# Performance work log

Measured on AMD Instinct MI355X. Metric: run time of the kernel, lower is better.

## Reference

```python
import jax, jax.numpy as jnp
import numpy as np

KS = {0: (6, 18), 1: (4, 12)}


def _build_modal_edges(feat, k_set):
    # feat: [N, C] -> H_modal [N, len(k_set)*N]
    N = feat.shape[0]
    f = feat / jnp.linalg.norm(feat, axis=1, keepdims=True).clip(1e-12)
    sim = f @ f.T  # [N, N] cosine similarity
    H_list = []
    cols_base = jnp.arange(N)
    for k in k_set:
        _, knn = jax.lax.top_k(sim, k + 1)  # [N, k+1]
        rows = knn.reshape(-1)
        cols = jnp.repeat(cols_base, k + 1)
        H = jnp.zeros((N, N), dtype=feat.dtype).at[rows, cols].set(1.0)
        H_list.append(H)
    return jnp.concatenate(H_list, axis=1)


def _build_incidence(feat1, feat2):
    # feat1/feat2: [N, C] (batch-mean features) -> H [2N, 5N]
    N = feat1.shape[0]
    H1 = _build_modal_edges(feat1, KS[0])  # [N, 2N]
    H2 = _build_modal_edges(feat2, KS[1])  # [N, 2N]
    E1, E2 = H1.shape[1], H2.shape[1]
    blk = jnp.concatenate([
        jnp.concatenate([H1, jnp.zeros((N, E2), H1.dtype)], axis=1),
        jnp.concatenate([jnp.zeros((N, E1), H2.dtype), H2], axis=1),
    ], axis=0)  # block_diag -> [2N, 4N]
    eye = jnp.eye(N, dtype=H1.dtype)
    H_inter = jnp.concatenate([eye, eye], axis=0)  # [2N, N]
    return jnp.concatenate([blk, H_inter], axis=1)  # [2N, 5N]


def _hgconv(x, H, W):
    # x: [B, 2N, Fin], H: [2N, E], W: [Fout, Fin] (torch Linear, no bias)
    x = jnp.einsum('bnf,of->bno', x, W)
    DV = H.sum(axis=1).clip(1.0)  # [2N]
    DE = H.sum(axis=0).clip(1.0)  # [E]
    H_norm = H / jnp.sqrt(DV)[:, None] / DE[None, :]
    A = H_norm @ H_norm.T  # [2N, 2N]
    x = jnp.einsum('nm,bmo->bno', A, x)
    return jax.nn.relu(x)


def setup_inputs() -> dict:
    key = jax.random.key(0)
    k1, k2, k3, k4 = jax.random.split(key, 4)
    B, N, C, Hd = 4, 2048, 64, 128
    feat_mod1 = jax.random.normal(k1, (B, N, C), dtype=jnp.float32)
    feat_mod2 = jax.random.normal(k2, (B, N, C), dtype=jnp.float32)
    # xavier_uniform bounds for [out, in]
    b1 = float(np.sqrt(6.0 / (Hd + C)))
    b2 = float(np.sqrt(6.0 / (Hd + Hd)))
    W1 = jax.random.uniform(k3, (Hd, C), minval=-b1, maxval=b1, dtype=jnp.float32)
    W2 = jax.random.uniform(k4, (Hd, Hd), minval=-b2, maxval=b2, dtype=jnp.float32)
    return {"feat_mod1": feat_mod1, "feat_mod2": feat_mod2, "W1": W1, "W2": W2}


def reference(feat_mod1, feat_mod2, W1, W2):
    B, N, _ = feat_mod1.shape
    H = jax.lax.stop_gradient(
        _build_incidence(feat_mod1.mean(axis=0), feat_mod2.mean(axis=0)))
    x = jnp.concatenate([feat_mod1, feat_mod2], axis=1)  # [B, 2N, C]
    x = _hgconv(x, H, W1)
    x = _hgconv(x, H, W2)
    return x[:, :N, :], x[:, N:, :]
```

## Files before the change

kernel.cpp:

```cpp
#include <hip/hip_runtime.h>
#include <math.h>

#define NN 2048
#define TWO_N 4096
#define BB 4
#define CC 64
#define HD 128
#define CANDCAP 32

typedef unsigned short u16;
typedef _Float16 h16;
union H4 { ushort4 u; h16 h[4]; };

__device__ __forceinline__ u16 f2bf(float x) {
    unsigned u = __float_as_uint(x);
    u += 0x7FFFu + ((u >> 16) & 1u);
    return (u16)(u >> 16);
}

__global__ void k_mean_norm(const float* __restrict__ f1, const float* __restrict__ f2,
                            const float* __restrict__ W1, const float* __restrict__ W2,
                            float* __restrict__ g32T, double* __restrict__ gR64,
                            u16* __restrict__ xh,
                            float* __restrict__ W1T, float* __restrict__ W2T,
                            int* __restrict__ DV) {
    int n = blockIdx.x;
    int m = blockIdx.y;
    int c = threadIdx.x;
    if (m == 0 && n < 64) DV[n * 64 + c] = 0;
    if (m == 1) {
        if (n < 128) {
            int idx = n * 64 + c;
            W1T[(size_t)(idx & 63) * HD + (idx >> 6)] = W1[idx];
        } else if (n < 384) {
            int idx = (n - 128) * 64 + c;
            W2T[(size_t)(idx & 127) * HD + (idx >> 7)] = W2[idx];
        }
    }
    const float* f = m ? f2 : f1;
    float xv[BB];
    double s = 0.0;
    for (int b = 0; b < BB; ++b) {
        float v = f[((size_t)(b * NN) + n) * CC + c];
        xv[b] = v; s += (double)v;
    }
    h16* xrow = (h16*)(xh + ((size_t)(m * NN + n)) * (BB * CC));
    for (int b = 0; b < BB; ++b) xrow[b * CC + c] = (h16)xv[b];
    double mean = s * 0.25;
    double sq = mean * mean;
    for (int d = 32; d >= 1; d >>= 1) sq += __shfl_xor(sq, d);
    double norm = sqrt(sq);
    if (norm < 1e-12) norm = 1e-12;
    double g = mean / norm;
    g32T[((size_t)m * CC + c) * NN + n] = (float)g;
    gR64[((size_t)m * NN + n) * CC + c] = g;
}

__global__ void __launch_bounds__(256)
k_sims(const float* __restrict__ g32T, u16* __restrict__ simsbf) {
    __shared__ float As[64 * 64];
    __shared__ float Bs[64 * 64];
    int m  = blockIdx.y;
    int bi = blockIdx.x >> 5, bj = blockIdx.x & 31;
    if (bi > bj) return;
    int i0 = bi * 64, j0 = bj * 64;
    const float* g = g32T + (size_t)m * CC * NN;
    int tid = threadIdx.x;
    #pragma unroll
    for (int q = 0; q < 16; ++q) {
        int idx = q * 256 + tid;
        int k = idx >> 6, r = idx & 63;
        As[k * 64 + r] = g[(size_t)k * NN + i0 + r];
        Bs[k * 64 + r] = g[(size_t)k * NN + j0 + r];
    }
    __syncthreads();
    int tr = tid >> 4, tc = tid & 15;
    float acc[4][4] = {{0.f}};
    #pragma unroll
    for (int k = 0; k < CC; ++k) {
        float4 a = *((const float4*)&As[k * 64 + (tr << 2)]);
        float4 b = *((const float4*)&Bs[k * 64 + (tc << 2)]);
        acc[0][0] += a.x * b.x; acc[0][1] += a.x * b.y; acc[0][2] += a.x * b.z; acc[0][3] += a.x * b.w;
        acc[1][0] += a.y * b.x; acc[1][1] += a.y * b.y; acc[1][2] += a.y * b.z; acc[1][3] += a.y * b.w;
        acc[2][0] += a.z * b.x; acc[2][1] += a.z * b.y; acc[2][2] += a.z * b.z; acc[2][3] += a.z * b.w;
        acc[3][0] += a.w * b.x; acc[3][1] += a.w * b.y; acc[3][2] += a.w * b.z; acc[3][3] += a.w * b.w;
    }
    __syncthreads();
    u16* Cs = (u16*)As;
    u16* srow = simsbf + (size_t)m * NN * NN;
    #pragma unroll
    for (int x = 0; x < 4; ++x) {
        ushort4 vd;
        vd.x = f2bf(acc[x][0]); vd.y = f2bf(acc[x][1]);
        vd.z = f2bf(acc[x][2]); vd.w = f2bf(acc[x][3]);
        *((ushort4*)&srow[(size_t)(i0 + (tr << 2) + x) * NN + j0 + (tc << 2)]) = vd;
        int cr = ((tr << 2) + x) * 66 + (tc << 2);
        Cs[cr + 0] = vd.x; Cs[cr + 1] = vd.y; Cs[cr + 2] = vd.z; Cs[cr + 3] = vd.w;
    }
    __syncthreads();
    #pragma unroll
    for (int q = 0; q < 4; ++q) {
        int idx = q * 256 + tid;
        int cc = idx >> 4, rr4 = (idx & 15) << 2;
        ushort4 vd;
        vd.x = Cs[(rr4 + 0) * 66 + cc];
        vd.y = Cs[(rr4 + 1) * 66 + cc];
        vd.z = Cs[(rr4 + 2) * 66 + cc];
        vd.w = Cs[(rr4 + 3) * 66 + cc];
        *((ushort4*)&srow[(size_t)(j0 + cc) * NN + i0 + rr4]) = vd;
    }
}

__global__ void __launch_bounds__(512)
k_selref(const u16* __restrict__ simsbf, const double* __restrict__ gR64,
         int* __restrict__ knn1, int* __restrict__ knn2, int* __restrict__ DV) {
    __shared__ int    candL[8][CANDCAP];
    __shared__ double dotsL[8][CANDCAP];
    int wave = threadIdx.x >> 6, lane = threadIdx.x & 63;
    int row = blockIdx.x * 8 + wave;
    int m = row >> 11, i = row & 2047;
    int K = m ? 13 : 19;
    const u16* s = simsbf + (size_t)m * NN * NN + (size_t)i * NN;
    float sv[32];
    #pragma unroll
    for (int q = 0; q < 4; ++q) {
        uint4 w = *((const uint4*)(s + q * 512 + (lane << 3)));
        sv[q*8+0] = __uint_as_float(w.x << 16);
        sv[q*8+1] = __uint_as_float(w.x & 0xFFFF0000u);
        sv[q*8+2] = __uint_as_float(w.y << 16);
        sv[q*8+3] = __uint_as_float(w.y & 0xFFFF0000u);
        sv[q*8+4] = __uint_as_float(w.z << 16);
        sv[q*8+5] = __uint_as_float(w.z & 0xFFFF0000u);
        sv[q*8+6] = __uint_as_float(w.w << 16);
        sv[q*8+7] = __uint_as_float(w.w & 0xFFFF0000u);
    }
    float lo = -1.01f, hi = 1.01f;
    for (int it = 0; it < 12; ++it) {
        float t = 0.5f * (lo + hi);
        int c = 0;
        #pragma unroll
        for (int r = 0; r < 32; ++r)
            c += __popcll(__ballot(sv[r] >= t));
        if (c >= K) lo = t; else hi = t;
    }
    float thr = lo - 6e-3f;
    unsigned long long ltmask = (lane == 0) ? 0ull : ((~0ull) >> (64 - lane));
    int base = 0;
    #pragma unroll
    for (int r = 0; r < 32; ++r) {
        int j = ((r >> 3) << 9) + (lane << 3) + (r & 7);
        bool p = sv[r] >= thr;
        unsigned long long mk = __ballot(p);
        int ofs = base + __popcll(mk & ltmask);
        if (p && ofs < CANDCAP) candL[wave][ofs] = j;
        base += __popcll(mk);
    }
    int cnt = (base < CANDCAP) ? base : CANDCAP;
    __syncthreads();
    const double* gm = gR64 + (size_t)m * NN * CC;
    double qc = gm[(size_t)i * CC + lane];
    int t4 = 0;
    for (; t4 + 3 < cnt; t4 += 4) {
        int j0c = candL[wave][t4 + 0], j1c = candL[wave][t4 + 1];
        int j2c = candL[wave][t4 + 2], j3c = candL[wave][t4 + 3];
        double p0 = qc * gm[(size_t)j0c * CC + lane];
        double p1 = qc * gm[(size_t)j1c * CC + lane];
        double p2 = qc * gm[(size_t)j2c * CC + lane];
        double p3 = qc * gm[(size_t)j3c * CC + lane];
        #pragma unroll
        for (int d = 32; d >= 1; d >>= 1) {
            p0 += __shfl_xor(p0, d); p1 += __shfl_xor(p1, d);
            p2 += __shfl_xor(p2, d); p3 += __shfl_xor(p3, d);
        }
        if (lane == 0) {
            dotsL[wave][t4 + 0] = p0; dotsL[wave][t4 + 1] = p1;
            dotsL[wave][t4 + 2] = p2; dotsL[wave][t4 + 3] = p3;
        }
    }
    for (; t4 < cnt; ++t4) {
        int j = candL[wave][t4];
        double p = qc * gm[(size_t)j * CC + lane];
        #pragma unroll
        for (int d = 32; d >= 1; d >>= 1) p += __shfl_xor(p, d);
        if (lane == 0) dotsL[wave][t4] = p;
    }
    __syncthreads();
    int* knn = m ? knn2 : knn1;
    if (lane < cnt) {
        double vt = dotsL[wave][lane]; int jt = candL[wave][lane];
        int rank = 0;
        for (int s2 = 0; s2 < cnt; ++s2) {
            double vs = dotsL[wave][s2]; int js = candL[wave][s2];
            if (vs > vt || (vs == vt && js < jt)) ++rank;
        }
        if (rank < K) {
            knn[(size_t)i * K + rank] = jt;
            int w = (rank < (m ? 5 : 7)) ? 2 : 1;
            atomicAdd(&DV[m ? NN + jt : jt], w);
        }
    }
}

__global__ void k_scan(const int* __restrict__ DV, int* __restrict__ offs,
                       int* __restrict__ cursor, float* __restrict__ dvisf) {
    int lane = threadIdx.x;
    int base = lane * 64;
    int s = 0;
    for (int q = 0; q < 64; ++q) s += DV[base + q];
    int x = s;
    for (int d = 1; d < 64; d <<= 1) {
        int y = __shfl_up(x, d);
        if (lane >= d) x += y;
    }
    int run = x - s;
    for (int q = 0; q < 64; ++q) {
        int v = base + q;
        offs[v] = run; cursor[v] = run;
        dvisf[v] = (float)(1.0 / sqrt((double)(DV[v] + 1)));
        run += DV[v];
    }
    if (lane == 63) offs[TWO_N] = run;
}

__global__ void k_fill(const int* __restrict__ knn1, const int* __restrict__ knn2,
                       int* __restrict__ cursor, int* __restrict__ entries) {
    int id = blockIdx.x * blockDim.x + threadIdx.x;
    const int M1 = NN * 19, M2 = NN * 13;
    if (id < M1) {
        int i = id / 19, t = id % 19;
        int v = knn1[id];
        int p = atomicAdd(&cursor[v], 1); entries[p] = NN + i;
        if (t < 7) { int p2 = atomicAdd(&cursor[v], 1); entries[p2] = i; }
    } else if (id < M1 + M2) {
        int id2 = id - M1;
        int i = id2 / 13, t = id2 % 13;
        int v = NN + knn2[id2];
        int p = atomicAdd(&cursor[v], 1); entries[p] = 3 * NN + i;
        if (t < 5) { int p2 = atomicAdd(&cursor[v], 1); entries[p2] = 2 * NN + i; }
    }
}

__global__ void k_edgeX(const u16* __restrict__ xh, const float* __restrict__ dvisf,
                        const int* __restrict__ knn1, const int* __restrict__ knn2,
                        u16* __restrict__ uh1) {
    int blk = blockIdx.x;
    int t = threadIdx.x;
    int off = t * 4;
    if (blk < NN) {
        int mv = 0; float wv = 0.f;
        if (t < 19) { mv = knn1[(size_t)blk * 19 + t]; wv = dvisf[mv]; }
        float a0=0,a1=0,a2=0,a3=0;
        #pragma unroll
        for (int q = 0; q < 7; ++q) {
            int mq = __shfl(mv, q); float wq = __shfl(wv, q);
            H4 hv; hv.u = *((const ushort4*)(xh + (size_t)mq * 256 + off));
            a0 += (float)hv.h[0]*wq; a1 += (float)hv.h[1]*wq;
            a2 += (float)hv.h[2]*wq; a3 += (float)hv.h[3]*wq;
        }
        { H4 ho; ho.h[0]=(h16)(a0*(1.f/49.f)); ho.h[1]=(h16)(a1*(1.f/49.f));
          ho.h[2]=(h16)(a2*(1.f/49.f)); ho.h[3]=(h16)(a3*(1.f/49.f));
          *((ushort4*)(uh1 + (size_t)blk * 256 + off)) = ho.u; }
        #pragma unroll
        for (int q = 7; q < 19; ++q) {
            int mq = __shfl(mv, q); float wq = __shfl(wv, q);
            H4 hv; hv.u = *((const ushort4*)(xh + (size_t)mq * 256 + off));
            a0 += (float)hv.h[0]*wq; a1 += (float)hv.h[1]*wq;
            a2 += (float)hv.h[2]*wq; a3 += (float)hv.h[3]*wq;
        }
        { H4 ho; ho.h[0]=(h16)(a0*(1.f/361.f)); ho.h[1]=(h16)(a1*(1.f/361.f));
          ho.h[2]=(h16)(a2*(1.f/361.f)); ho.h[3]=(h16)(a3*(1.f/361.f));
          *((ushort4*)(uh1 + (size_t)(NN + blk) * 256 + off)) = ho.u; }
    } else {
        int i = blk - NN;
        int mv = 0; float wv = 0.f;
        if (t < 13) { mv = knn2[(size_t)i * 13 + t]; wv = dvisf[NN + mv]; }
        float a0=0,a1=0,a2=0,a3=0;
        #pragma unroll
        for (int q = 0; q < 5; ++q) {
            int mq = __shfl(mv, q); float wq = __shfl(wv, q);
            H4 hv; hv.u = *((const ushort4*)(xh + (size_t)(NN + mq) * 256 + off));
            a0 += (float)hv.h[0]*wq; a1 += (float)hv.h[1]*wq;
            a2 += (float)hv.h[2]*wq; a3 += (float)hv.h[3]*wq;
        }
        { H4 ho; ho.h[0]=(h16)(a0*(1.f/25.f)); ho.h[1]=(h16)(a1*(1.f/25.f));
          ho.h[2]=(h16)(a2*(1.f/25.f)); ho.h[3]=(h16)(a3*(1.f/25.f));
          *((ushort4*)(uh1 + (size_t)(2 * NN + i) * 256 + off)) = ho.u; }
        #pragma unroll
        for (int q = 5; q < 13; ++q) {
            int mq = __shfl(mv, q); float wq = __shfl(wv, q);
            H4 hv; hv.u = *((const ushort4*)(xh + (size_t)(NN + mq) * 256 + off));
            a0 += (float)hv.h[0]*wq; a1 += (float)hv.h[1]*wq;
            a2 += (float)hv.h[2]*wq; a3 += (float)hv.h[3]*wq;
        }
        { H4 ho; ho.h[0]=(h16)(a0*(1.f/169.f)); ho.h[1]=(h16)(a1*(1.f/169.f));
          ho.h[2]=(h16)(a2*(1.f/169.f)); ho.h[3]=(h16)(a3*(1.f/169.f));
          *((ushort4*)(uh1 + (size_t)(3 * NN + i) * 256 + off)) = ho.u; }
    }
}

__global__ void k_node1(const u16* __restrict__ uh1,
                        const float* __restrict__ f1, const float* __restrict__ f2,
                        const float* __restrict__ dvisf,
                        const int* __restrict__ offs, const int* __restrict__ entries,
                        u16* __restrict__ aggxh) {
    int v = blockIdx.x;
    int l6 = threadIdx.x;
    int b = l6 >> 4, f4i = l6 & 15;
    int s = offs[v], e_end = offs[v + 1];
    float A0[4] = {0,0,0,0}, A1[4] = {0,0,0,0};
    float A2[4] = {0,0,0,0}, A3[4] = {0,0,0,0};
    int p = s;
    for (; p + 3 < e_end; p += 4) {
        H4 h0, h1, h2, h3;
        h0.u = *((const ushort4*)(uh1 + (size_t)entries[p+0] * 256 + l6 * 4));
        h1.u = *((const ushort4*)(uh1 + (size_t)entries[p+1] * 256 + l6 * 4));
        h2.u = *((const ushort4*)(uh1 + (size_t)entries[p+2] * 256 + l6 * 4));
        h3.u = *((const ushort4*)(uh1 + (size_t)entries[p+3] * 256 + l6 * 4));
        #pragma unroll
        for (int j = 0; j < 4; ++j) {
            A0[j] += (float)h0.h[j]; A1[j] += (float)h1.h[j];
            A2[j] += (float)h2.h[j]; A3[j] += (float)h3.h[j];
        }
    }
    for (; p < e_end; ++p) {
        H4 h0; h0.u = *((const ushort4*)(uh1 + (size_t)entries[p] * 256 + l6 * 4));
        #pragma unroll
        for (int j = 0; j < 4; ++j) A0[j] += (float)h0.h[j];
    }
    float r[4];
    #pragma unroll
    for (int j = 0; j < 4; ++j) r[j] = (A0[j] + A1[j]) + (A2[j] + A3[j]);
    int partner = (v < NN) ? v + NN : v - NN;
    float w0 = dvisf[v], w1 = dvisf[partner];
    const float4* x1 = (const float4*)f1;
    const float4* x2 = (const float4*)f2;
    float4 xv = (v < NN) ? x1[((size_t)(b * NN) + v) * 16 + f4i]
                         : x2[((size_t)(b * NN) + (v - NN)) * 16 + f4i];
    float4 xp = (partner < NN) ? x1[((size_t)(b * NN) + partner) * 16 + f4i]
                               : x2[((size_t)(b * NN) + (partner - NN)) * 16 + f4i];
    r[0] += 0.25f * (xv.x * w0 + xp.x * w1);
    r[1] += 0.25f * (xv.y * w0 + xp.y * w1);
    r[2] += 0.25f * (xv.z * w0 + xp.z * w1);
    r[3] += 0.25f * (xv.w * w0 + xp.w * w1);
    H4 ho;
    #pragma unroll
    for (int j = 0; j < 4; ++j) ho.h[j] = (h16)(r[j] * w0);
    *((ushort4*)(aggxh + (size_t)v * 256 + l6 * 4)) = ho.u;
}

__global__ void __launch_bounds__(256)
k_gemm12(const u16* __restrict__ aggxh,
         const float* __restrict__ W1T, const float* __restrict__ W2T,
         u16* __restrict__ yh) {
    __shared__ float wT[64 * 132];
    __shared__ float xT[64 * 33];
    __shared__ float zT[128 * 33];
    int tid = threadIdx.x;
    int bid = blockIdx.x;
    int v0 = bid * 8, g0 = bid * 32;
    #pragma unroll
    for (int p = 0; p < 32; ++p) {
        int idx = p * 256 + tid;
        wT[(idx >> 7) * 132 + (idx & 127)] = W1T[idx];
    }
    #pragma unroll
    for (int it = 0; it < 2; ++it) {
        int item = it * 256 + tid;
        int vl = item >> 6, l6 = item & 63;
        int b = l6 >> 4, c4 = (l6 & 15) << 2;
        H4 hv; hv.u = *((const ushort4*)(aggxh + (size_t)(v0 + vl) * 256 + l6 * 4));
        int rloc = vl * 4 + b;
        #pragma unroll
        for (int j = 0; j < 4; ++j) xT[(c4 + j) * 33 + rloc] = (float)hv.h[j];
    }
    __syncthreads();
    int tr = tid >> 5, tc = tid & 31;
    int r0 = tr * 4, c0 = tc * 4;
    {
        float acc[4][4] = {{0.f}};
        #pragma unroll
        for (int k = 0; k < CC; ++k) {
            float xr0 = xT[k*33 + r0+0], xr1 = xT[k*33 + r0+1];
            float xr2 = xT[k*33 + r0+2], xr3 = xT[k*33 + r0+3];
            float4 w = *((const float4*)&wT[k * 132 + c0]);
            acc[0][0]+=xr0*w.x; acc[0][1]+=xr0*w.y; acc[0][2]+=xr0*w.z; acc[0][3]+=xr0*w.w;
            acc[1][0]+=xr1*w.x; acc[1][1]+=xr1*w.y; acc[1][2]+=xr1*w.z; acc[1][3]+=xr1*w.w;
            acc[2][0]+=xr2*w.x; acc[2][1]+=xr2*w.y; acc[2][2]+=xr2*w.z; acc[2][3]+=xr2*w.w;
            acc[3][0]+=xr3*w.x; acc[3][1]+=xr3*w.y; acc[3][2]+=xr3*w.z; acc[3][3]+=xr3*w.w;
        }
        #pragma unroll
        for (int i = 0; i < 4; ++i)
            #pragma unroll
            for (int j = 0; j < 4; ++j)
                zT[(c0 + j) * 33 + r0 + i] = fmaxf(acc[i][j], 0.f);
    }
    float acc2[4][4] = {{0.f}};
    for (int kc = 0; kc < 2; ++kc) {
        __syncthreads();
        #pragma unroll
        for (int p = 0; p < 32; ++p) {
            int idx = p * 256 + tid;
            int k = idx >> 7, c = idx & 127;
            wT[k * 132 + c] = W2T[(size_t)(kc * 64 + k) * HD + c];
        }
        __syncthreads();
        #pragma unroll
        for (int k = 0; k < 64; ++k) {
            int kk = kc * 64 + k;
            float zr0 = zT[kk*33 + r0+0], zr1 = zT[kk*33 + r0+1];
            float zr2 = zT[kk*33 + r0+2], zr3 = zT[kk*33 + r0+3];
            float4 w = *((const float4*)&wT[k * 132 + c0]);
            acc2[0][0]+=zr0*w.x; acc2[0][1]+=zr0*w.y; acc2[0][2]+=zr0*w.z; acc2[0][3]+=zr0*w.w;
            acc2[1][0]+=zr1*w.x; acc2[1][1]+=zr1*w.y; acc2[1][2]+=zr1*w.z; acc2[1][3]+=zr1*w.w;
            acc2[2][0]+=zr2*w.x; acc2[2][1]+=zr2*w.y; acc2[2][2]+=zr2*w.z; acc2[2][3]+=zr2*w.w;
            acc2[3][0]+=zr3*w.x; acc2[3][1]+=zr3*w.y; acc2[3][2]+=zr3*w.z; acc2[3][3]+=zr3*w.w;
        }
    }
    #pragma unroll
    for (int i = 0; i < 4; ++i) {
        H4 ho;
        ho.h[0] = (h16)acc2[i][0]; ho.h[1] = (h16)acc2[i][1];
        ho.h[2] = (h16)acc2[i][2]; ho.h[3] = (h16)acc2[i][3];
        *((ushort4*)(yh + (size_t)(g0 + r0 + i) * HD + c0)) = ho.u;
    }
}

__global__ void k_edge2(const u16* __restrict__ yh, const float* __restrict__ dvisf,
                        const int* __restrict__ knn1, const int* __restrict__ knn2,
                        u16* __restrict__ uh2) {
    __shared__ int mem[19];
    __shared__ float wv[19];
    int blk = blockIdx.x;
    int t = threadIdx.x;
    int off = t * 4;
    if (blk < NN) {
        if (t < 19) { int v = knn1[(size_t)blk * 19 + t]; mem[t] = v; wv[t] = dvisf[v]; }
        __syncthreads();
        float a0=0,a1=0,a2=0,a3=0;
        #pragma unroll
        for (int q = 0; q < 7; ++q) {
            float w = wv[q];
            H4 hv; hv.u = *((const ushort4*)(yh + (size_t)mem[q] * 512 + off));
            a0 += (float)hv.h[0]*w; a1 += (float)hv.h[1]*w;
            a2 += (float)hv.h[2]*w; a3 += (float)hv.h[3]*w;
        }
        { H4 ho; ho.h[0]=(h16)(a0*(1.f/49.f)); ho.h[1]=(h16)(a1*(1.f/49.f));
          ho.h[2]=(h16)(a2*(1.f/49.f)); ho.h[3]=(h16)(a3*(1.f/49.f));
          *((ushort4*)(uh2 + (size_t)blk * 512 + off)) = ho.u; }
        #pragma unroll
        for (int q = 7; q < 19; ++q) {
            float w = wv[q];
            H4 hv; hv.u = *((const ushort4*)(yh + (size_t)mem[q] * 512 + off));
            a0 += (float)hv.h[0]*w; a1 += (float)hv.h[1]*w;
            a2 += (float)hv.h[2]*w; a3 += (float)hv.h[3]*w;
        }
        { H4 ho; ho.h[0]=(h16)(a0*(1.f/361.f)); ho.h[1]=(h16)(a1*(1.f/361.f));
          ho.h[2]=(h16)(a2*(1.f/361.f)); ho.h[3]=(h16)(a3*(1.f/361.f));
          *((ushort4*)(uh2 + (size_t)(NN + blk) * 512 + off)) = ho.u; }
    } else {
        int i = blk - NN;
        if (t < 13) { int v = NN + knn2[(size_t)i * 13 + t]; mem[t] = v; wv[t] = dvisf[v]; }
        __syncthreads();
        float a0=0,a1=0,a2=0,a3=0;
        #pragma unroll
        for (int q = 0; q < 5; ++q) {
            float w = wv[q];
            H4 hv; hv.u = *((const ushort4*)(yh + (size_t)mem[q] * 512 + off));
            a0 += (float)hv.h[0]*w; a1 += (float)hv.h[1]*w;
            a2 += (float)hv.h[2]*w; a3 += (float)hv.h[3]*w;
        }
        { H4 ho; ho.h[0]=(h16)(a0*(1.f/25.f)); ho.h[1]=(h16)(a1*(1.f/25.f));
          ho.h[2]=(h16)(a2*(1.f/25.f)); ho.h[3]=(h16)(a3*(1.f/25.f));
          *((ushort4*)(uh2 + (size_t)(2 * NN + i) * 512 + off)) = ho.u; }
        #pragma unroll
        for (int q = 5; q < 13; ++q) {
            float w = wv[q];
            H4 hv; hv.u = *((const ushort4*)(yh + (size_t)mem[q] * 512 + off));
            a0 += (float)hv.h[0]*w; a1 += (float)hv.h[1]*w;
            a2 += (float)hv.h[2]*w; a3 += (float)hv.h[3]*w;
        }
        { H4 ho; ho.h[0]=(h16)(a0*(1.f/169.f)); ho.h[1]=(h16)(a1*(1.f/169.f));
          ho.h[2]=(h16)(a2*(1.f/169.f)); ho.h[3]=(h16)(a3*(1.f/169.f));
          *((ushort4*)(uh2 + (size_t)(3 * NN + i) * 512 + off)) = ho.u; }
    }
}

__global__ void k_node2(const u16* __restrict__ uh2, const u16* __restrict__ yh,
                        const float* __restrict__ dvisf,
                        const int* __restrict__ offs, const int* __restrict__ entries,
                        float* __restrict__ out) {
    int v = blockIdx.x;
    int t = threadIdx.x;
    int off = t * 4;
    int s = offs[v], e_end = offs[v + 1];
    float A0[4] = {0,0,0,0}, A1[4] = {0,0,0,0};
    float A2[4] = {0,0,0,0}, A3[4] = {0,0,0,0};
    int p = s;
    for (; p + 3 < e_end; p += 4) {
        H4 h0, h1, h2, h3;
        h0.u = *((const ushort4*)(uh2 + (size_t)entries[p+0] * 512 + off));
        h1.u = *((const ushort4*)(uh2 + (size_t)entries[p+1] * 512 + off));
        h2.u = *((const ushort4*)(uh2 + (size_t)entries[p+2] * 512 + off));
        h3.u = *((const ushort4*)(uh2 + (size_t)entries[p+3] * 512 + off));
        #pragma unroll
        for (int j = 0; j < 4; ++j) {
            A0[j] += (float)h0.h[j]; A1[j] += (float)h1.h[j];
            A2[j] += (float)h2.h[j]; A3[j] += (float)h3.h[j];
        }
    }
    for (; p < e_end; ++p) {
        H4 h0; h0.u = *((const ushort4*)(uh2 + (size_t)entries[p] * 512 + off));
        #pragma unroll
        for (int j = 0; j < 4; ++j) A0[j] += (float)h0.h[j];
    }
    float r[4];
    #pragma unroll
    for (int j = 0; j < 4; ++j) r[j] = (A0[j] + A1[j]) + (A2[j] + A3[j]);
    int partner = (v < NN) ? v + NN : v - NN;
    float w0 = dvisf[v], w1 = dvisf[partner];
    H4 yv, yp;
    yv.u = *((const ushort4*)(yh + (size_t)v * 512 + off));
    yp.u = *((const ushort4*)(yh + (size_t)partner * 512 + off));
    #pragma unroll
    for (int j = 0; j < 4; ++j) {
        r[j] += 0.25f * ((float)yv.h[j] * w0 + (float)yp.h[j] * w1);
        r[j] = fmaxf(r[j] * w0, 0.f);
    }
    int b = t >> 5, f4i = t & 31;
    size_t o4;
    if (v < NN) o4 = ((size_t)(b * NN + v)) * 32 + f4i;
    else        o4 = (size_t)BB * NN * 32 + ((size_t)(b * NN + (v - NN))) * 32 + f4i;
    ((float4*)out)[o4] = make_float4(r[0], r[1], r[2], r[3]);
}

extern "C" void kernel_launch(void* const* d_in, const int* in_sizes, int n_in,
                              void* d_out, int out_size, void* d_ws, size_t ws_size,
                              hipStream_t stream) {
    const float* f1 = (const float*)d_in[0];
    const float* f2 = (const float*)d_in[1];
    const float* W1 = (const float*)d_in[2];
    const float* W2 = (const float*)d_in[3];
    float* out = (float*)d_out;

    char* ws = (char*)d_ws;
    size_t off = 0;
    auto alloc = [&](size_t bytes) -> void* {
        void* p = ws + off;
        off = (off + bytes + 255) & ~(size_t)255;
        return p;
    };
    float*  g32T   = (float*)alloc((size_t)2 * CC * NN * 4);
    double* gR64   = (double*)alloc((size_t)2 * NN * CC * 8);
    u16*    simsbf = (u16*)alloc((size_t)2 * NN * NN * 2);
    u16*    xh     = (u16*)alloc((size_t)TWO_N * BB * CC * 2);
    u16*    uh1    = (u16*)alloc((size_t)4 * NN * BB * CC * 2);
    u16*    aggxh  = (u16*)alloc((size_t)TWO_N * BB * CC * 2);
    u16*    yh     = (u16*)alloc((size_t)TWO_N * BB * HD * 2);
    u16*    uh2    = (u16*)alloc((size_t)4 * NN * BB * HD * 2);
    float*  W1T    = (float*)alloc((size_t)CC * HD * 4);
    float*  W2T    = (float*)alloc((size_t)HD * HD * 4);
    float*  dvisf  = (float*)alloc((size_t)TWO_N * 4);
    int*    knn1   = (int*)alloc((size_t)NN * 19 * 4);
    int*    knn2   = (int*)alloc((size_t)NN * 13 * 4);
    int*    DV     = (int*)alloc((size_t)TWO_N * 4);
    int*    offs   = (int*)alloc((size_t)(TWO_N + 1) * 4);
    int*    cursor = (int*)alloc((size_t)TWO_N * 4);
    int*    entries= (int*)alloc((size_t)(NN * 26 + NN * 18) * 4);

    k_mean_norm<<<dim3(NN, 2), 64, 0, stream>>>(f1, f2, W1, W2, g32T, gR64,
                                                xh, W1T, W2T, DV);
    k_sims<<<dim3(32 * 32, 2), 256, 0, stream>>>(g32T, simsbf);
    k_selref<<<TWO_N / 8, 512, 0, stream>>>(simsbf, gR64, knn1, knn2, DV);
    k_scan<<<1, 64, 0, stream>>>(DV, offs, cursor, dvisf);
    k_fill<<<(NN * 19 + NN * 13 + 255) / 256, 256, 0, stream>>>(knn1, knn2, cursor, entries);

    k_edgeX<<<2 * NN, 64, 0, stream>>>(xh, dvisf, knn1, knn2, uh1);
    k_node1<<<TWO_N, 64, 0, stream>>>(uh1, f1, f2, dvisf, offs, entries, aggxh);
    k_gemm12<<<(BB * TWO_N) / 32, 256, 0, stream>>>(aggxh, W1T, W2T, yh);

    k_edge2<<<2 * NN, 128, 0, stream>>>(yh, dvisf, knn1, knn2, uh2);
    k_node2<<<TWO_N, 128, 0, stream>>>(uh2, yh, dvisf, offs, entries, out);
}
```

Measured before the change: 188.8 us.

## Fuse graph-construction kernels into one persistent kernel with grid barriers

Replaces six separate launches (mean/norm, similarity GEMM, top-k selection, scan, fill, first edge aggregation) with a single persistent kernel of 384 blocks that separates phases with hierarchical atomic grid barriers. The aim is to remove per-launch overhead and the idle tails between the small dependent kernels. In exchange, phases run at a fixed occupancy, fill and edge aggregation now share a phase, and correctness depends on all blocks being co-resident and on the magic-flag handshake for barrier reset.

```diff
diff --git a/kernel.cpp b/kernel.cpp
--- a/kernel.cpp
+++ b/kernel.cpp
@@ -8,9 +8,41 @@
 #define HD 128
 #define CANDCAP 32
 
+#define NBLK 384
+#define NTHR 512
+#define NWAVES (NBLK * 8)
+
+#define MAGIC0 0x13579BDF
+#define MAGIC1 0x2468ACE1
+
 typedef unsigned short u16;
 typedef _Float16 h16;
 union H4 { ushort4 u; h16 h[4]; };
+
+struct BarMem {
+    int flag[16];
+    int sub[12][8][16];
+    int master[12][16];
+};
+#define BAR_ZERO_DWORDS (12 * 8 * 16 + 12 * 16)
+
+__device__ __forceinline__ void gbar(BarMem* B, int idx) {
+    __syncthreads();
+    if (threadIdx.x == 0) {
+        int line = blockIdx.x & 7;
+        int a = __hip_atomic_fetch_add(&B->sub[idx][line][0], 1,
+                                       __ATOMIC_ACQ_REL, __HIP_MEMORY_SCOPE_AGENT);
+        if (a == (NBLK / 8) - 1)
+            __hip_atomic_fetch_add(&B->master[idx][0], 1,
+                                   __ATOMIC_ACQ_REL, __HIP_MEMORY_SCOPE_AGENT);
+        while (__hip_atomic_load(&B->master[idx][0],
+                                 __ATOMIC_RELAXED, __HIP_MEMORY_SCOPE_AGENT) != 8)
+            __builtin_amdgcn_s_sleep(8);
+        (void)__hip_atomic_load(&B->master[idx][0],
+                                __ATOMIC_ACQUIRE, __HIP_MEMORY_SCOPE_AGENT);
+    }
+    __syncthreads();
+}
 
 __device__ __forceinline__ u16 f2bf(float x) {
     unsigned u = __float_as_uint(x);
@@ -18,283 +50,337 @@
     return (u16)(u >> 16);
 }
 
-__global__ void k_mean_norm(const float* __restrict__ f1, const float* __restrict__ f2,
-                            const float* __restrict__ W1, const float* __restrict__ W2,
-                            float* __restrict__ g32T, double* __restrict__ gR64,
-                            u16* __restrict__ xh,
-                            float* __restrict__ W1T, float* __restrict__ W2T,
-                            int* __restrict__ DV) {
-    int n = blockIdx.x;
-    int m = blockIdx.y;
-    int c = threadIdx.x;
-    if (m == 0 && n < 64) DV[n * 64 + c] = 0;
-    if (m == 1) {
-        if (n < 128) {
-            int idx = n * 64 + c;
-            W1T[(size_t)(idx & 63) * HD + (idx >> 6)] = W1[idx];
-        } else if (n < 384) {
-            int idx = (n - 128) * 64 + c;
-            W2T[(size_t)(idx & 127) * HD + (idx >> 7)] = W2[idx];
-        }
-    }
-    const float* f = m ? f2 : f1;
-    float xv[BB];
-    double s = 0.0;
-    for (int b = 0; b < BB; ++b) {
-        float v = f[((size_t)(b * NN) + n) * CC + c];
-        xv[b] = v; s += (double)v;
-    }
-    h16* xrow = (h16*)(xh + ((size_t)(m * NN + n)) * (BB * CC));
-    for (int b = 0; b < BB; ++b) xrow[b * CC + c] = (h16)xv[b];
-    double mean = s * 0.25;
-    double sq = mean * mean;
-    for (int d = 32; d >= 1; d >>= 1) sq += __shfl_xor(sq, d);
-    double norm = sqrt(sq);
-    if (norm < 1e-12) norm = 1e-12;
-    double g = mean / norm;
-    g32T[((size_t)m * CC + c) * NN + n] = (float)g;
-    gR64[((size_t)m * NN + n) * CC + c] = g;
-}
-
-__global__ void __launch_bounds__(256)
-k_sims(const float* __restrict__ g32T, u16* __restrict__ simsbf) {
-    __shared__ float As[64 * 64];
-    __shared__ float Bs[64 * 64];
-    int m  = blockIdx.y;
-    int bi = blockIdx.x >> 5, bj = blockIdx.x & 31;
-    if (bi > bj) return;
-    int i0 = bi * 64, j0 = bj * 64;
-    const float* g = g32T + (size_t)m * CC * NN;
-    int tid = threadIdx.x;
-    #pragma unroll
-    for (int q = 0; q < 16; ++q) {
-        int idx = q * 256 + tid;
-        int k = idx >> 6, r = idx & 63;
-        As[k * 64 + r] = g[(size_t)k * NN + i0 + r];
-        Bs[k * 64 + r] = g[(size_t)k * NN + j0 + r];
-    }
-    __syncthreads();
-    int tr = tid >> 4, tc = tid & 15;
-    float acc[4][4] = {{0.f}};
-    #pragma unroll
-    for (int k = 0; k < CC; ++k) {
-        float4 a = *((const float4*)&As[k * 64 + (tr << 2)]);
-        float4 b = *((const float4*)&Bs[k * 64 + (tc << 2)]);
-        acc[0][0] += a.x * b.x; acc[0][1] += a.x * b.y; acc[0][2] += a.x * b.z; acc[0][3] += a.x * b.w;
-        acc[1][0] += a.y * b.x; acc[1][1] += a.y * b.y; acc[1][2] += a.y * b.z; acc[1][3] += a.y * b.w;
-        acc[2][0] += a.z * b.x; acc[2][1] += a.z * b.y; acc[2][2] += a.z * b.z; acc[2][3] += a.z * b.w;
-        acc[3][0] += a.w * b.x; acc[3][1] += a.w * b.y; acc[3][2] += a.w * b.z; acc[3][3] += a.w * b.w;
-    }
-    __syncthreads();
-    u16* Cs = (u16*)As;
-    u16* srow = simsbf + (size_t)m * NN * NN;
-    #pragma unroll
-    for (int x = 0; x < 4; ++x) {
-        ushort4 vd;
-        vd.x = f2bf(acc[x][0]); vd.y = f2bf(acc[x][1]);
-        vd.z = f2bf(acc[x][2]); vd.w = f2bf(acc[x][3]);
-        *((ushort4*)&srow[(size_t)(i0 + (tr << 2) + x) * NN + j0 + (tc << 2)]) = vd;
-        int cr = ((tr << 2) + x) * 66 + (tc << 2);
-        Cs[cr + 0] = vd.x; Cs[cr + 1] = vd.y; Cs[cr + 2] = vd.z; Cs[cr + 3] = vd.w;
-    }
-    __syncthreads();
-    #pragma unroll
-    for (int q = 0; q < 4; ++q) {
-        int idx = q * 256 + tid;
-        int cc = idx >> 4, rr4 = (idx & 15) << 2;
-        ushort4 vd;
-        vd.x = Cs[(rr4 + 0) * 66 + cc];
-        vd.y = Cs[(rr4 + 1) * 66 + cc];
-        vd.z = Cs[(rr4 + 2) * 66 + cc];
-        vd.w = Cs[(rr4 + 3) * 66 + cc];
-        *((ushort4*)&srow[(size_t)(j0 + cc) * NN + i0 + rr4]) = vd;
-    }
-}
-
-__global__ void __launch_bounds__(512)
-k_selref(const u16* __restrict__ simsbf, const double* __restrict__ gR64,
-         int* __restrict__ knn1, int* __restrict__ knn2, int* __restrict__ DV) {
-    __shared__ int    candL[8][CANDCAP];
-    __shared__ double dotsL[8][CANDCAP];
-    int wave = threadIdx.x >> 6, lane = threadIdx.x & 63;
-    int row = blockIdx.x * 8 + wave;
-    int m = row >> 11, i = row & 2047;
-    int K = m ? 13 : 19;
-    const u16* s = simsbf + (size_t)m * NN * NN + (size_t)i * NN;
-    float sv[32];
-    #pragma unroll
-    for (int q = 0; q < 4; ++q) {
-        uint4 w = *((const uint4*)(s + q * 512 + (lane << 3)));
-        sv[q*8+0] = __uint_as_float(w.x << 16);
-        sv[q*8+1] = __uint_as_float(w.x & 0xFFFF0000u);
-        sv[q*8+2] = __uint_as_float(w.y << 16);
-        sv[q*8+3] = __uint_as_float(w.y & 0xFFFF0000u);
-        sv[q*8+4] = __uint_as_float(w.z << 16);
-        sv[q*8+5] = __uint_as_float(w.z & 0xFFFF0000u);
-        sv[q*8+6] = __uint_as_float(w.w << 16);
-        sv[q*8+7] = __uint_as_float(w.w & 0xFFFF0000u);
-    }
-    float lo = -1.01f, hi = 1.01f;
-    for (int it = 0; it < 12; ++it) {
-        float t = 0.5f * (lo + hi);
-        int c = 0;
-        #pragma unroll
-        for (int r = 0; r < 32; ++r)
-            c += __popcll(__ballot(sv[r] >= t));
-        if (c >= K) lo = t; else hi = t;
-    }
-    float thr = lo - 6e-3f;
-    unsigned long long ltmask = (lane == 0) ? 0ull : ((~0ull) >> (64 - lane));
-    int base = 0;
-    #pragma unroll
-    for (int r = 0; r < 32; ++r) {
-        int j = ((r >> 3) << 9) + (lane << 3) + (r & 7);
-        bool p = sv[r] >= thr;
-        unsigned long long mk = __ballot(p);
-        int ofs = base + __popcll(mk & ltmask);
-        if (p && ofs < CANDCAP) candL[wave][ofs] = j;
-        base += __popcll(mk);
-    }
-    int cnt = (base < CANDCAP) ? base : CANDCAP;
-    __syncthreads();
-    const double* gm = gR64 + (size_t)m * NN * CC;
-    double qc = gm[(size_t)i * CC + lane];
-    int t4 = 0;
-    for (; t4 + 3 < cnt; t4 += 4) {
-        int j0c = candL[wave][t4 + 0], j1c = candL[wave][t4 + 1];
-        int j2c = candL[wave][t4 + 2], j3c = candL[wave][t4 + 3];
-        double p0 = qc * gm[(size_t)j0c * CC + lane];
-        double p1 = qc * gm[(size_t)j1c * CC + lane];
-        double p2 = qc * gm[(size_t)j2c * CC + lane];
-        double p3 = qc * gm[(size_t)j3c * CC + lane];
-        #pragma unroll
-        for (int d = 32; d >= 1; d >>= 1) {
-            p0 += __shfl_xor(p0, d); p1 += __shfl_xor(p1, d);
-            p2 += __shfl_xor(p2, d); p3 += __shfl_xor(p3, d);
-        }
-        if (lane == 0) {
-            dotsL[wave][t4 + 0] = p0; dotsL[wave][t4 + 1] = p1;
-            dotsL[wave][t4 + 2] = p2; dotsL[wave][t4 + 3] = p3;
-        }
-    }
-    for (; t4 < cnt; ++t4) {
-        int j = candL[wave][t4];
-        double p = qc * gm[(size_t)j * CC + lane];
-        #pragma unroll
-        for (int d = 32; d >= 1; d >>= 1) p += __shfl_xor(p, d);
-        if (lane == 0) dotsL[wave][t4] = p;
-    }
-    __syncthreads();
-    int* knn = m ? knn2 : knn1;
-    if (lane < cnt) {
-        double vt = dotsL[wave][lane]; int jt = candL[wave][lane];
-        int rank = 0;
-        for (int s2 = 0; s2 < cnt; ++s2) {
-            double vs = dotsL[wave][s2]; int js = candL[wave][s2];
-            if (vs > vt || (vs == vt && js < jt)) ++rank;
-        }
-        if (rank < K) {
-            knn[(size_t)i * K + rank] = jt;
-            int w = (rank < (m ? 5 : 7)) ? 2 : 1;
-            atomicAdd(&DV[m ? NN + jt : jt], w);
-        }
-    }
-}
-
-__global__ void k_scan(const int* __restrict__ DV, int* __restrict__ offs,
-                       int* __restrict__ cursor, float* __restrict__ dvisf) {
-    int lane = threadIdx.x;
-    int base = lane * 64;
-    int s = 0;
-    for (int q = 0; q < 64; ++q) s += DV[base + q];
-    int x = s;
-    for (int d = 1; d < 64; d <<= 1) {
-        int y = __shfl_up(x, d);
-        if (lane >= d) x += y;
-    }
-    int run = x - s;
-    for (int q = 0; q < 64; ++q) {
-        int v = base + q;
-        offs[v] = run; cursor[v] = run;
-        dvisf[v] = (float)(1.0 / sqrt((double)(DV[v] + 1)));
-        run += DV[v];
-    }
-    if (lane == 63) offs[TWO_N] = run;
-}
-
-__global__ void k_fill(const int* __restrict__ knn1, const int* __restrict__ knn2,
-                       int* __restrict__ cursor, int* __restrict__ entries) {
-    int id = blockIdx.x * blockDim.x + threadIdx.x;
-    const int M1 = NN * 19, M2 = NN * 13;
-    if (id < M1) {
-        int i = id / 19, t = id % 19;
-        int v = knn1[id];
-        int p = atomicAdd(&cursor[v], 1); entries[p] = NN + i;
-        if (t < 7) { int p2 = atomicAdd(&cursor[v], 1); entries[p2] = i; }
-    } else if (id < M1 + M2) {
-        int id2 = id - M1;
-        int i = id2 / 13, t = id2 % 13;
-        int v = NN + knn2[id2];
-        int p = atomicAdd(&cursor[v], 1); entries[p] = 3 * NN + i;
-        if (t < 5) { int p2 = atomicAdd(&cursor[v], 1); entries[p2] = 2 * NN + i; }
-    }
-}
-
-__global__ void k_edgeX(const u16* __restrict__ xh, const float* __restrict__ dvisf,
-                        const int* __restrict__ knn1, const int* __restrict__ knn2,
-                        u16* __restrict__ uh1) {
-    int blk = blockIdx.x;
-    int t = threadIdx.x;
-    int off = t * 4;
-    if (blk < NN) {
-        int mv = 0; float wv = 0.f;
-        if (t < 19) { mv = knn1[(size_t)blk * 19 + t]; wv = dvisf[mv]; }
-        float a0=0,a1=0,a2=0,a3=0;
-        #pragma unroll
-        for (int q = 0; q < 7; ++q) {
-            int mq = __shfl(mv, q); float wq = __shfl(wv, q);
-            H4 hv; hv.u = *((const ushort4*)(xh + (size_t)mq * 256 + off));
-            a0 += (float)hv.h[0]*wq; a1 += (float)hv.h[1]*wq;
-            a2 += (float)hv.h[2]*wq; a3 += (float)hv.h[3]*wq;
-        }
-        { H4 ho; ho.h[0]=(h16)(a0*(1.f/49.f)); ho.h[1]=(h16)(a1*(1.f/49.f));
-          ho.h[2]=(h16)(a2*(1.f/49.f)); ho.h[3]=(h16)(a3*(1.f/49.f));
-          *((ushort4*)(uh1 + (size_t)blk * 256 + off)) = ho.u; }
-        #pragma unroll
-        for (int q = 7; q < 19; ++q) {
-            int mq = __shfl(mv, q); float wq = __shfl(wv, q);
-            H4 hv; hv.u = *((const ushort4*)(xh + (size_t)mq * 256 + off));
-            a0 += (float)hv.h[0]*wq; a1 += (float)hv.h[1]*wq;
-            a2 += (float)hv.h[2]*wq; a3 += (float)hv.h[3]*wq;
-        }
-        { H4 ho; ho.h[0]=(h16)(a0*(1.f/361.f)); ho.h[1]=(h16)(a1*(1.f/361.f));
-          ho.h[2]=(h16)(a2*(1.f/361.f)); ho.h[3]=(h16)(a3*(1.f/361.f));
-          *((ushort4*)(uh1 + (size_t)(NN + blk) * 256 + off)) = ho.u; }
+__global__ void __launch_bounds__(NTHR, 4)
+k_graph(const float* __restrict__ f1, const float* __restrict__ f2,
+        const float* __restrict__ W1, const float* __restrict__ W2,
+        BarMem* __restrict__ bar,
+        float* __restrict__ g32T, double* __restrict__ gR64,
+        u16* __restrict__ simsbf, u16* __restrict__ xh, u16* __restrict__ uh1,
+        float* __restrict__ W1T, float* __restrict__ W2T,
+        float* __restrict__ dvisf,
+        int* __restrict__ knn1, int* __restrict__ knn2,
+        int* __restrict__ DV, int* __restrict__ offs,
+        int* __restrict__ cursor, int* __restrict__ entries) {
+    __shared__ __align__(16) char SMEM[65536];
+
+    const int tid  = threadIdx.x;
+    const int bid  = blockIdx.x;
+    const int lane = tid & 63;
+    const int wid  = tid >> 6;
+    const int gwave = bid * 8 + wid;
+    const int team = tid >> 8;
+    const int tid2 = tid & 255;
+
+    if (bid == 0) {
+        int* bz = &bar->sub[0][0][0];
+        for (int i = tid; i < BAR_ZERO_DWORDS; i += NTHR) bz[i] = 0;
+        __syncthreads();
+        if (tid == 0) {
+            __hip_atomic_store(&bar->flag[0], MAGIC0, __ATOMIC_RELEASE, __HIP_MEMORY_SCOPE_AGENT);
+            __hip_atomic_store(&bar->flag[1], MAGIC1, __ATOMIC_RELEASE, __HIP_MEMORY_SCOPE_AGENT);
+        }
     } else {
-        int i = blk - NN;
-        int mv = 0; float wv = 0.f;
-        if (t < 13) { mv = knn2[(size_t)i * 13 + t]; wv = dvisf[NN + mv]; }
-        float a0=0,a1=0,a2=0,a3=0;
-        #pragma unroll
-        for (int q = 0; q < 5; ++q) {
-            int mq = __shfl(mv, q); float wq = __shfl(wv, q);
-            H4 hv; hv.u = *((const ushort4*)(xh + (size_t)(NN + mq) * 256 + off));
-            a0 += (float)hv.h[0]*wq; a1 += (float)hv.h[1]*wq;
-            a2 += (float)hv.h[2]*wq; a3 += (float)hv.h[3]*wq;
-        }
-        { H4 ho; ho.h[0]=(h16)(a0*(1.f/25.f)); ho.h[1]=(h16)(a1*(1.f/25.f));
-          ho.h[2]=(h16)(a2*(1.f/25.f)); ho.h[3]=(h16)(a3*(1.f/25.f));
-          *((ushort4*)(uh1 + (size_t)(2 * NN + i) * 256 + off)) = ho.u; }
-        #pragma unroll
-        for (int q = 5; q < 13; ++q) {
-            int mq = __shfl(mv, q); float wq = __shfl(wv, q);
-            H4 hv; hv.u = *((const ushort4*)(xh + (size_t)(NN + mq) * 256 + off));
-            a0 += (float)hv.h[0]*wq; a1 += (float)hv.h[1]*wq;
-            a2 += (float)hv.h[2]*wq; a3 += (float)hv.h[3]*wq;
-        }
-        { H4 ho; ho.h[0]=(h16)(a0*(1.f/169.f)); ho.h[1]=(h16)(a1*(1.f/169.f));
-          ho.h[2]=(h16)(a2*(1.f/169.f)); ho.h[3]=(h16)(a3*(1.f/169.f));
-          *((ushort4*)(uh1 + (size_t)(3 * NN + i) * 256 + off)) = ho.u; }
+        if (tid == 0) {
+            while (__hip_atomic_load(&bar->flag[0], __ATOMIC_RELAXED, __HIP_MEMORY_SCOPE_AGENT) != MAGIC0 ||
+                   __hip_atomic_load(&bar->flag[1], __ATOMIC_RELAXED, __HIP_MEMORY_SCOPE_AGENT) != MAGIC1)
+                __builtin_amdgcn_s_sleep(8);
+            (void)__hip_atomic_load(&bar->flag[0], __ATOMIC_ACQUIRE, __HIP_MEMORY_SCOPE_AGENT);
+        }
+        __syncthreads();
+    }
+
+    {
+        int gid = bid * NTHR + tid;
+        if (gid < HD * CC) {
+            int c = gid >> 6, k = gid & 63;
+            W1T[(size_t)k * HD + c] = W1[gid];
+        }
+        if (gid < HD * HD) {
+            int c = gid >> 7, k = gid & 127;
+            W2T[(size_t)k * HD + c] = W2[gid];
+        }
+        if (gid < TWO_N) DV[gid] = 0;
+
+        for (int rowt = gwave; rowt < TWO_N; rowt += NWAVES) {
+            int m = rowt >> 11, n = rowt & 2047;
+            const float* f = m ? f2 : f1;
+            float xv[BB];
+            double s = 0.0;
+            for (int b = 0; b < BB; ++b) {
+                float v = f[((size_t)(b * NN) + n) * CC + lane];
+                xv[b] = v; s += (double)v;
+            }
+            h16* xrow = (h16*)(xh + ((size_t)(m * NN + n)) * (BB * CC));
+            for (int b = 0; b < BB; ++b) xrow[b * CC + lane] = (h16)xv[b];
+            double mean = s * 0.25;
+            double sq = mean * mean;
+            for (int d = 32; d >= 1; d >>= 1) sq += __shfl_xor(sq, d);
+            double norm = sqrt(sq);
+            if (norm < 1e-12) norm = 1e-12;
+            double gg = mean / norm;
+            g32T[((size_t)m * CC + lane) * NN + n] = (float)gg;
+            gR64[((size_t)m * NN + n) * CC + lane] = gg;
+        }
+    }
+    gbar(bar, 0);
+
+    {
+        for (int itr = 0; itr < 2; ++itr) {
+            int tile = bid * 2 + team + itr * (NBLK * 2);
+            bool act = tile < 1056;
+            int m = 0, bi = 0, bj = 0;
+            if (act) {
+                m = tile >= 528 ? 1 : 0;
+                int r = tile - m * 528;
+                while (r >= 32 - bi) { r -= 32 - bi; ++bi; }
+                bj = bi + r;
+            }
+            float* As = (float*)(SMEM + (size_t)team * 32768);
+            float* Bs = As + 4096;
+            int i0 = bi * 64, j0 = bj * 64;
+            const float* g = g32T + (size_t)m * CC * NN;
+            if (act) {
+                #pragma unroll
+                for (int q = 0; q < 16; ++q) {
+                    int idx = q * 256 + tid2;
+                    int k = idx >> 6, rr = idx & 63;
+                    As[k * 64 + rr] = g[(size_t)k * NN + i0 + rr];
+                    Bs[k * 64 + rr] = g[(size_t)k * NN + j0 + rr];
+                }
+            }
+            __syncthreads();
+            float acc[4][4] = {{0.f}};
+            int tr = tid2 >> 4, tc = tid2 & 15;
+            if (act) {
+                #pragma unroll
+                for (int k = 0; k < CC; ++k) {
+                    float4 a = *((const float4*)&As[k * 64 + (tr << 2)]);
+                    float4 b = *((const float4*)&Bs[k * 64 + (tc << 2)]);
+                    acc[0][0] += a.x * b.x; acc[0][1] += a.x * b.y; acc[0][2] += a.x * b.z; acc[0][3] += a.x * b.w;
+                    acc[1][0] += a.y * b.x; acc[1][1] += a.y * b.y; acc[1][2] += a.y * b.z; acc[1][3] += a.y * b.w;
+                    acc[2][0] += a.z * b.x; acc[2][1] += a.z * b.y; acc[2][2] += a.z * b.z; acc[2][3] += a.z * b.w;
+                    acc[3][0] += a.w * b.x; acc[3][1] += a.w * b.y; acc[3][2] += a.w * b.z; acc[3][3] += a.w * b.w;
+                }
+            }
+            __syncthreads();
+            u16* Cs = (u16*)As;
+            u16* srow = simsbf + (size_t)m * NN * NN;
+            if (act) {
+                #pragma unroll
+                for (int x = 0; x < 4; ++x) {
+                    ushort4 vd;
+                    vd.x = f2bf(acc[x][0]); vd.y = f2bf(acc[x][1]);
+                    vd.z = f2bf(acc[x][2]); vd.w = f2bf(acc[x][3]);
+                    *((ushort4*)&srow[(size_t)(i0 + (tr << 2) + x) * NN + j0 + (tc << 2)]) = vd;
+                    int cr = ((tr << 2) + x) * 66 + (tc << 2);
+                    Cs[cr + 0] = vd.x; Cs[cr + 1] = vd.y;
+                    Cs[cr + 2] = vd.z; Cs[cr + 3] = vd.w;
+                }
+            }
+            __syncthreads();
+            if (act) {
+                #pragma unroll
+                for (int q = 0; q < 4; ++q) {
+                    int idx = q * 256 + tid2;
+                    int cc = idx >> 4, rr4 = (idx & 15) << 2;
+                    ushort4 vd;
+                    vd.x = Cs[(rr4 + 0) * 66 + cc];
+                    vd.y = Cs[(rr4 + 1) * 66 + cc];
+                    vd.z = Cs[(rr4 + 2) * 66 + cc];
+                    vd.w = Cs[(rr4 + 3) * 66 + cc];
+                    *((ushort4*)&srow[(size_t)(j0 + cc) * NN + i0 + rr4]) = vd;
+                }
+            }
+            __syncthreads();
+        }
+    }
+    gbar(bar, 1);
+
+    {
+        int* candL = (int*)(SMEM + (size_t)wid * 384);
+        double* dotsL = (double*)(SMEM + (size_t)wid * 384 + 128);
+        for (int row = gwave; row < TWO_N; row += NWAVES) {
+            int m = row >> 11, i = row & 2047;
+            int K = m ? 13 : 19;
+            const u16* s = simsbf + (size_t)m * NN * NN + (size_t)i * NN;
+            float sv[32];
+            #pragma unroll
+            for (int q = 0; q < 4; ++q) {
+                uint4 w = *((const uint4*)(s + q * 512 + (lane << 3)));
+                sv[q*8+0] = __uint_as_float(w.x << 16);
+                sv[q*8+1] = __uint_as_float(w.x & 0xFFFF0000u);
+                sv[q*8+2] = __uint_as_float(w.y << 16);
+                sv[q*8+3] = __uint_as_float(w.y & 0xFFFF0000u);
+                sv[q*8+4] = __uint_as_float(w.z << 16);
+                sv[q*8+5] = __uint_as_float(w.z & 0xFFFF0000u);
+                sv[q*8+6] = __uint_as_float(w.w << 16);
+                sv[q*8+7] = __uint_as_float(w.w & 0xFFFF0000u);
+            }
+            float lo = -1.01f, hi = 1.01f;
+            for (int it = 0; it < 12; ++it) {
+                float t = 0.5f * (lo + hi);
+                int c = 0;
+                #pragma unroll
+                for (int r = 0; r < 32; ++r)
+                    c += __popcll(__ballot(sv[r] >= t));
+                if (c >= K) lo = t; else hi = t;
+            }
+            float thr = lo - 6e-3f;
+            unsigned long long ltmask = (lane == 0) ? 0ull : ((~0ull) >> (64 - lane));
+            int base = 0;
+            #pragma unroll
+            for (int r = 0; r < 32; ++r) {
+                int j = ((r >> 3) << 9) + (lane << 3) + (r & 7);
+                bool p = sv[r] >= thr;
+                unsigned long long mk = __ballot(p);
+                int ofs = base + __popcll(mk & ltmask);
+                if (p && ofs < CANDCAP) candL[ofs] = j;
+                base += __popcll(mk);
+            }
+            int cnt = (base < CANDCAP) ? base : CANDCAP;
+            __threadfence_block();
+            const double* gm = gR64 + (size_t)m * NN * CC;
+            double qc = gm[(size_t)i * CC + lane];
+            int t4 = 0;
+            for (; t4 + 3 < cnt; t4 += 4) {
+                int j0c = candL[t4 + 0], j1c = candL[t4 + 1];
+                int j2c = candL[t4 + 2], j3c = candL[t4 + 3];
+                double p0 = qc * gm[(size_t)j0c * CC + lane];
+                double p1 = qc * gm[(size_t)j1c * CC + lane];
+                double p2 = qc * gm[(size_t)j2c * CC + lane];
+                double p3 = qc * gm[(size_t)j3c * CC + lane];
+                #pragma unroll
+                for (int d = 32; d >= 1; d >>= 1) {
+                    p0 += __shfl_xor(p0, d); p1 += __shfl_xor(p1, d);
+                    p2 += __shfl_xor(p2, d); p3 += __shfl_xor(p3, d);
+                }
+                if (lane == 0) {
+                    dotsL[t4 + 0] = p0; dotsL[t4 + 1] = p1;
+                    dotsL[t4 + 2] = p2; dotsL[t4 + 3] = p3;
+                }
+            }
+            for (; t4 < cnt; ++t4) {
+                int j = candL[t4];
+                double p = qc * gm[(size_t)j * CC + lane];
+                #pragma unroll
+                for (int d = 32; d >= 1; d >>= 1) p += __shfl_xor(p, d);
+                if (lane == 0) dotsL[t4] = p;
+            }
+            __threadfence_block();
+            int* knn = m ? knn2 : knn1;
+            if (lane < cnt) {
+                double vt = dotsL[lane]; int jt = candL[lane];
+                int rank = 0;
+                for (int s2 = 0; s2 < cnt; ++s2) {
+                    double vs = dotsL[s2]; int js = candL[s2];
+                    if (vs > vt || (vs == vt && js < jt)) ++rank;
+                }
+                if (rank < K) {
+                    knn[(size_t)i * K + rank] = jt;
+                    int w = (rank < (m ? 5 : 7)) ? 2 : 1;
+                    atomicAdd(&DV[m ? NN + jt : jt], w);
+                }
+            }
+            __threadfence_block();
+        }
+    }
+    gbar(bar, 2);
+
+    if (bid == 0 && tid < 64) {
+        int ln = tid;
+        int base = ln * 64;
+        int s = 0;
+        for (int q = 0; q < 64; ++q) s += DV[base + q];
+        int x = s;
+        for (int d = 1; d < 64; d <<= 1) {
+            int y = __shfl_up(x, d);
+            if (ln >= d) x += y;
+        }
+        int run = x - s;
+        for (int q = 0; q < 64; ++q) {
+            int v = base + q;
+            offs[v] = run; cursor[v] = run;
+            dvisf[v] = (float)(1.0 / sqrt((double)(DV[v] + 1)));
+            run += DV[v];
+        }
+        if (ln == 63) offs[TWO_N] = run;
+    }
+    gbar(bar, 3);
+
+    {
+        int gid = bid * NTHR + tid;
+        const int M1 = NN * 19, M2 = NN * 13;
+        if (gid < M1) {
+            int i = gid / 19, t = gid % 19;
+            int v = knn1[gid];
+            int p = atomicAdd(&cursor[v], 1); entries[p] = NN + i;
+            if (t < 7) { int p2 = atomicAdd(&cursor[v], 1); entries[p2] = i; }
+        } else if (gid < M1 + M2) {
+            int id2 = gid - M1;
+            int i = id2 / 13, t = id2 % 13;
+            int v = NN + knn2[id2];
+            int p = atomicAdd(&cursor[v], 1); entries[p] = 3 * NN + i;
+            if (t < 5) { int p2 = atomicAdd(&cursor[v], 1); entries[p2] = 2 * NN + i; }
+        }
+
+        int off = lane * 4;
+        for (int pt = gwave; pt < TWO_N; pt += NWAVES) {
+            if (pt < NN) {
+                int mv = 0; float wv = 0.f;
+                if (lane < 19) { mv = knn1[(size_t)pt * 19 + lane]; wv = dvisf[mv]; }
+                float a0=0,a1=0,a2=0,a3=0;
+                #pragma unroll
+                for (int q = 0; q < 7; ++q) {
+                    int mq = __shfl(mv, q); float wq = __shfl(wv, q);
+                    H4 hv; hv.u = *((const ushort4*)(xh + (size_t)mq * 256 + off));
+                    a0 += (float)hv.h[0]*wq; a1 += (float)hv.h[1]*wq;
+                    a2 += (float)hv.h[2]*wq; a3 += (float)hv.h[3]*wq;
+                }
+                { H4 ho; ho.h[0]=(h16)(a0*(1.f/49.f)); ho.h[1]=(h16)(a1*(1.f/49.f));
+                  ho.h[2]=(h16)(a2*(1.f/49.f)); ho.h[3]=(h16)(a3*(1.f/49.f));
+                  *((ushort4*)(uh1 + (size_t)pt * 256 + off)) = ho.u; }
+                #pragma unroll
+                for (int q = 7; q < 19; ++q) {
+                    int mq = __shfl(mv, q); float wq = __shfl(wv, q);
+                    H4 hv; hv.u = *((const ushort4*)(xh + (size_t)mq * 256 + off));
+                    a0 += (float)hv.h[0]*wq; a1 += (float)hv.h[1]*wq;
+                    a2 += (float)hv.h[2]*wq; a3 += (float)hv.h[3]*wq;
+                }
+                { H4 ho; ho.h[0]=(h16)(a0*(1.f/361.f)); ho.h[1]=(h16)(a1*(1.f/361.f));
+                  ho.h[2]=(h16)(a2*(1.f/361.f)); ho.h[3]=(h16)(a3*(1.f/361.f));
+                  *((ushort4*)(uh1 + (size_t)(NN + pt) * 256 + off)) = ho.u; }
+            } else {
+                int i = pt - NN;
+                int mv = 0; float wv = 0.f;
+                if (lane < 13) { mv = knn2[(size_t)i * 13 + lane]; wv = dvisf[NN + mv]; }
+                float a0=0,a1=0,a2=0,a3=0;
+                #pragma unroll
+                for (int q = 0; q < 5; ++q) {
+                    int mq = __shfl(mv, q); float wq = __shfl(wv, q);
+                    H4 hv; hv.u = *((const ushort4*)(xh + (size_t)(NN + mq) * 256 + off));
+                    a0 += (float)hv.h[0]*wq; a1 += (float)hv.h[1]*wq;
+                    a2 += (float)hv.h[2]*wq; a3 += (float)hv.h[3]*wq;
+                }
+                { H4 ho; ho.h[0]=(h16)(a0*(1.f/25.f)); ho.h[1]=(h16)(a1*(1.f/25.f));
+                  ho.h[2]=(h16)(a2*(1.f/25.f)); ho.h[3]=(h16)(a3*(1.f/25.f));
+                  *((ushort4*)(uh1 + (size_t)(2 * NN + i) * 256 + off)) = ho.u; }
+                #pragma unroll
+                for (int q = 5; q < 13; ++q) {
+                    int mq = __shfl(mv, q); float wq = __shfl(wv, q);
+                    H4 hv; hv.u = *((const ushort4*)(xh + (size_t)(NN + mq) * 256 + off));
+                    a0 += (float)hv.h[0]*wq; a1 += (float)hv.h[1]*wq;
+                    a2 += (float)hv.h[2]*wq; a3 += (float)hv.h[3]*wq;
+                }
+                { H4 ho; ho.h[0]=(h16)(a0*(1.f/169.f)); ho.h[1]=(h16)(a1*(1.f/169.f));
+                  ho.h[2]=(h16)(a2*(1.f/169.f)); ho.h[3]=(h16)(a3*(1.f/169.f));
+                  *((ushort4*)(uh1 + (size_t)(3 * NN + i) * 256 + off)) = ho.u; }
+            }
+        }
+    }
+
+    if (bid == 0 && tid == 0) {
+        __hip_atomic_store(&bar->flag[0], 0, __ATOMIC_RELEASE, __HIP_MEMORY_SCOPE_AGENT);
+        __hip_atomic_store(&bar->flag[1], 0, __ATOMIC_RELEASE, __HIP_MEMORY_SCOPE_AGENT);
     }
 }
 
@@ -549,6 +635,7 @@
         off = (off + bytes + 255) & ~(size_t)255;
         return p;
     };
+    BarMem* bar    = (BarMem*)alloc(sizeof(BarMem));
     float*  g32T   = (float*)alloc((size_t)2 * CC * NN * 4);
     double* gR64   = (double*)alloc((size_t)2 * NN * CC * 8);
     u16*    simsbf = (u16*)alloc((size_t)2 * NN * NN * 2);
@@ -567,17 +654,12 @@
     int*    cursor = (int*)alloc((size_t)TWO_N * 4);
     int*    entries= (int*)alloc((size_t)(NN * 26 + NN * 18) * 4);
 
-    k_mean_norm<<<dim3(NN, 2), 64, 0, stream>>>(f1, f2, W1, W2, g32T, gR64,
-                                                xh, W1T, W2T, DV);
-    k_sims<<<dim3(32 * 32, 2), 256, 0, stream>>>(g32T, simsbf);
-    k_selref<<<TWO_N / 8, 512, 0, stream>>>(simsbf, gR64, knn1, knn2, DV);
-    k_scan<<<1, 64, 0, stream>>>(DV, offs, cursor, dvisf);
-    k_fill<<<(NN * 19 + NN * 13 + 255) / 256, 256, 0, stream>>>(knn1, knn2, cursor, entries);
-
-    k_edgeX<<<2 * NN, 64, 0, stream>>>(xh, dvisf, knn1, knn2, uh1);
+    k_graph<<<dim3(NBLK), dim3(NTHR), 0, stream>>>(
+        f1, f2, W1, W2, bar, g32T, gR64, simsbf, xh, uh1,
+        W1T, W2T, dvisf, knn1, knn2, DV, offs, cursor, entries);
+
     k_node1<<<TWO_N, 64, 0, stream>>>(uh1, f1, f2, dvisf, offs, entries, aggxh);
     k_gemm12<<<(BB * TWO_N) / 32, 256, 0, stream>>>(aggxh, W1T, W2T, yh);
-
     k_edge2<<<2 * NN, 128, 0, stream>>>(yh, dvisf, knn1, knn2, uh2);
     k_node2<<<TWO_N, 128, 0, stream>>>(uh2, yh, dvisf, offs, entries, out);
 }
```

Result: slower. 266.8 us (+41.3%).
